# Performance work log

Hardware: AMD Instinct MI355X
Metric: run time of the kernel (lower is better)

## Reference

```python
import jax, jax.numpy as jnp
import numpy as np

BITS = 4
N_PACK = 32 // BITS  # int32 compression
GROUPSIZE = 128
MASK = (1 << BITS) - 1


def _unpack_int32(q, axis):
    """Unpack int32 tensor into N_PACK low-bit values along `axis`.
    Element j*N_PACK+e comes from bits [BITS*e, BITS*(e+1)) of packed word j."""
    parts = [ (q >> (BITS * e)) & MASK for e in range(N_PACK) ]
    u = jnp.stack(parts, axis=axis + 1)  # (..., P, N_PACK, ...)
    shape = list(q.shape)
    shape[axis] = shape[axis] * N_PACK
    return u.reshape(shape)


def setup_inputs() -> dict:
    key = jax.random.key(0)
    k1, k2, k3, k4, k5 = jax.random.split(key, 5)
    in_f, out_f = 4096, 12288
    tokens = 8192
    n_groups = in_f // GROUPSIZE  # 32
    x = jax.random.normal(k1, (tokens, in_f), dtype=jnp.float32)
    scales = jax.random.uniform(k2, (n_groups, out_f), dtype=jnp.float32) * 0.01 + 1e-3
    bias = jax.random.normal(k3, (out_f,), dtype=jnp.float32)
    qweight = jax.random.randint(k4, (in_f // N_PACK, out_f), jnp.iinfo(jnp.int32).min, jnp.iinfo(jnp.int32).max, dtype=jnp.int32)
    qzeros = jax.random.randint(k5, (n_groups, out_f // N_PACK), jnp.iinfo(jnp.int32).min, jnp.iinfo(jnp.int32).max, dtype=jnp.int32)
    return {"x": x, "scales": scales, "bias": bias, "qweight": qweight, "qzeros": qzeros}


def reference(x, scales, bias, qweight, qzeros):
    in_f = qweight.shape[0] * N_PACK
    out_f = qweight.shape[1]
    n_groups = scales.shape[0]
    # Unpack 4-bit weights along input-channel axis: (in_f, out_f), values 0..15
    w_int = _unpack_int32(qweight, axis=0).astype(scales.dtype)
    # Unpack zero points along output-channel axis; optimum format stores zp-1
    zp = (_unpack_int32(qzeros, axis=1) + 1).astype(scales.dtype)  # (n_groups, out_f)
    # Per-group dequant: group g covers input channels [g*GROUPSIZE, (g+1)*GROUPSIZE)
    w = (w_int.reshape(n_groups, GROUPSIZE, out_f) - zp[:, None, :]) * scales[:, None, :]
    w = w.reshape(in_f, out_f)
    # Linear: y = x @ W^T with W = w.T, i.e. x @ w
    return x @ w + bias
```

## Files before the change

### kernel.cpp

```cpp
#include <hip/hip_runtime.h>
#include <hip/hip_bf16.h>


typedef __attribute__((ext_vector_type(8))) short short8;
typedef __attribute__((ext_vector_type(4))) float f32x4;

__device__ __forceinline__ short f2bf(float f) {
  unsigned u = __float_as_uint(f);
  u += 0x7fffu + ((u >> 16) & 1u);
  return (short)(u >> 16);
}

__device__ __forceinline__ void gload_lds16(const void* g, void* l) {
  __builtin_amdgcn_global_load_lds(
      (const __attribute__((address_space(1))) void*)g,
      (__attribute__((address_space(3))) void*)l,
      16, 0, 0);
}

__device__ __forceinline__ void bar() {
  asm volatile("" ::: "memory");
  __builtin_amdgcn_s_barrier();
  asm volatile("" ::: "memory");
}
__device__ __forceinline__ void wait_vm8() {
  asm volatile("s_waitcnt vmcnt(8)" ::: "memory");
}
__device__ __forceinline__ void wait_vm4() {
  asm volatile("s_waitcnt vmcnt(4)" ::: "memory");
}
__device__ __forceinline__ void wait_vm0() {
  asm volatile("s_waitcnt vmcnt(0)" ::: "memory");
}

__global__ __launch_bounds__(256) void dequant_kernel(
    const int* __restrict__ qweight, const int* __restrict__ qzeros,
    const float* __restrict__ scales, short* __restrict__ Wt,
    int in_f, int out_f) {
  __shared__ __align__(16) short T[64][72];
  const int n0 = blockIdx.x * 64;
  const int k0 = blockIdx.y * 64;
  const int t = threadIdx.x;
  const int nl = t & 63;
  const int kw = t >> 6;
  const int n = n0 + nl;
  const int g = k0 >> 7;
  const float sc = scales[(size_t)g * out_f + n];
  const int zpw = qzeros[(size_t)g * (out_f >> 3) + (n >> 3)];
  const float zp = (float)(((zpw >> ((n & 7) * 4)) & 15) + 1);
  const float zs = zp * sc;
#pragma unroll
  for (int rr = 0; rr < 2; ++rr) {
    const int kwi = kw + rr * 4;
    const int w = qweight[(size_t)((k0 >> 3) + kwi) * out_f + n];
    short8 v;
#pragma unroll
    for (int e = 0; e < 8; ++e) {
      float f = (float)((w >> (4 * e)) & 15) * sc - zs;
      v[e] = f2bf(f);
    }
    *(short8*)&T[nl][kwi * 8] = v;
  }
  __syncthreads();
#pragma unroll
  for (int rr = 0; rr < 2; ++rr) {
    const int c = rr * 256 + t;
    const int row = c >> 3, ch = c & 7;
    *(short8*)&Wt[(size_t)(n0 + row) * in_f + k0 + ch * 8] =
        *(const short8*)&T[row][ch * 8];
  }
}

__global__ __launch_bounds__(256) void cvt_kernel(
    const float* __restrict__ x, short* __restrict__ xb, long n8) {
  long i = (long)blockIdx.x * blockDim.x + threadIdx.x;
  if (i >= n8) return;
  const float* src = x + i * 8;
  float4 a = *(const float4*)src;
  float4 b = *(const float4*)(src + 4);
  short8 v;
  v[0] = f2bf(a.x); v[1] = f2bf(a.y); v[2] = f2bf(a.z); v[3] = f2bf(a.w);
  v[4] = f2bf(b.x); v[5] = f2bf(b.y); v[6] = f2bf(b.z); v[7] = f2bf(b.w);
  *(short8*)(xb + i * 8) = v;
}

#define GBM 256
#define GBN 256

__global__ __launch_bounds__(512, 2) void gemm256_kernel(
    const short* __restrict__ A, const short* __restrict__ Bt,
    const float* __restrict__ bias, float* __restrict__ C,
    int M, int N, int K) {
  __shared__ __align__(16) char lds[4][32768];
  const int tid = threadIdx.x;
  const int nbx = N / GBN;
  const int nwg = gridDim.x;
  int bid = blockIdx.x;
  if ((nwg & 7) == 0) bid = (bid & 7) * (nwg >> 3) + (bid >> 3);
  const int bm = (bid / nbx) * GBM;
  const int bn = (bid % nbx) * GBN;

  const int wid = tid >> 6, lane = tid & 63;
  const int wr = wid >> 2, wc = wid & 3;
  const int lrow = lane & 15;
  const int lq = lane >> 4;

  const int P = K >> 5;

  int offA[2][4], offB[4];
#pragma unroll
  for (int mh = 0; mh < 2; ++mh)
#pragma unroll
    for (int i = 0; i < 4; ++i) {
      const int row = wr * 128 + mh * 64 + i * 16 + lrow;
      const int s = lq ^ ((row >> 1) & 3);
      offA[mh][i] = row * 64 + s * 16;
    }
#pragma unroll
  for (int j = 0; j < 4; ++j) {
    const int row = wc * 64 + j * 16 + lrow;
    const int s = lq ^ ((row >> 1) & 3);
    offB[j] = 16384 + row * 64 + s * 16;
  }

  const int c0 = tid, c1 = tid + 512;
  const int rA0 = c0 >> 2, qA0 = (c0 & 3) ^ ((rA0 >> 1) & 3);
  const int rA1 = c1 >> 2, qA1 = (c1 & 3) ^ ((rA1 >> 1) & 3);
  const short* srcA0 = A + (size_t)(bm + rA0) * K + qA0 * 8;
  const short* srcA1 = A + (size_t)(bm + rA1) * K + qA1 * 8;
  const short* srcB0 = Bt + (size_t)(bn + rA0) * K + qA0 * 8;
  const short* srcB1 = Bt + (size_t)(bn + rA1) * K + qA1 * 8;
  const int dA0 = c0 * 16, dA1 = c1 * 16;
  const int dB0 = 16384 + c0 * 16, dB1 = 16384 + c1 * 16;

  auto STAGE = [&](int slot, int h) {
    const int kof = h * 32;
    char* sb = &lds[slot][0];
    gload_lds16(srcA0 + kof, sb + dA0);
    gload_lds16(srcA1 + kof, sb + dA1);
    gload_lds16(srcB0 + kof, sb + dB0);
    gload_lds16(srcB1 + kof, sb + dB1);
  };

  f32x4 acc[8][4] = {};

  auto PHASE = [&](int p, bool doStage) {
    const char* sb = &lds[p & 3][0];
    short8 bf[4], af[4];
#pragma unroll
    for (int j = 0; j < 4; ++j) bf[j] = *(const short8*)(sb + offB[j]);
#pragma unroll
    for (int i = 0; i < 4; ++i) af[i] = *(const short8*)(sb + offA[0][i]);
    if (doStage) STAGE((p + 3) & 3, p + 3);
    __builtin_amdgcn_s_setprio(1);
#pragma unroll
    for (int i = 0; i < 4; ++i)
#pragma unroll
      for (int j = 0; j < 4; ++j)
        acc[i][j] = __builtin_amdgcn_mfma_f32_16x16x32_bf16(
            af[i], bf[j], acc[i][j], 0, 0, 0);
    __builtin_amdgcn_s_setprio(0);
    short8 af2[4];
#pragma unroll
    for (int i = 0; i < 4; ++i) af2[i] = *(const short8*)(sb + offA[1][i]);
    __builtin_amdgcn_s_setprio(1);
#pragma unroll
    for (int i = 0; i < 4; ++i)
#pragma unroll
      for (int j = 0; j < 4; ++j)
        acc[4 + i][j] = __builtin_amdgcn_mfma_f32_16x16x32_bf16(
            af2[i], bf[j], acc[4 + i][j], 0, 0, 0);
    __builtin_amdgcn_s_setprio(0);
  };

  STAGE(0, 0);
  STAGE(1, 1);
  STAGE(2, 2);

  for (int p = 0; p <= P - 4; ++p) {
    wait_vm8();
    bar();
    PHASE(p, true);
  }
  wait_vm8(); bar(); PHASE(P - 3, false);
  wait_vm4(); bar(); PHASE(P - 2, false);
  wait_vm0(); bar(); PHASE(P - 1, false);

  const int crow0 = bm + wr * 128 + (lane >> 4) * 4;
  const int ccol0 = bn + wc * 64 + (lane & 15);
#pragma unroll
  for (int j = 0; j < 4; ++j) {
    const float bv = bias[ccol0 + j * 16];
#pragma unroll
    for (int i = 0; i < 8; ++i) {
#pragma unroll
      for (int r = 0; r < 4; ++r) {
        C[(size_t)(crow0 + i * 16 + r) * N + ccol0 + j * 16] =
            acc[i][j][r] + bv;
      }
    }
  }
}

#define BM 128
#define BN 128
#define BK 64

template <bool A_BF16>
__global__ __launch_bounds__(256) void gemm_bias_kernel(
    const void* __restrict__ Av, const short* __restrict__ Bt,
    const float* __restrict__ bias, float* __restrict__ C,
    int M, int N, int K) {
  __shared__ __align__(16) short As[BM * BK];
  __shared__ __align__(16) short Bs[BN * BK];
  const int tid = threadIdx.x;
  const int bm = blockIdx.y * BM;
  const int bn = blockIdx.x * BN;
  const int wid = tid >> 6, lane = tid & 63;
  const int wr = wid >> 1, wc = wid & 1;
  const int lrow = lane & 15;
  const int lk = (lane >> 4) * 8;

  f32x4 acc[4][4] = {};

  for (int kt = 0; kt < K; kt += BK) {
    if constexpr (A_BF16) {
      const short* A = (const short*)Av;
#pragma unroll
      for (int r = 0; r < 4; ++r) {
        const int c = r * 256 + tid;
        const int row = c >> 3, ch = c & 7;
        gload_lds16(A + (size_t)(bm + row) * K + kt + ch * 8,
                    (char*)As + c * 16);
      }
    } else {
      const float* A = (const float*)Av;
#pragma unroll
      for (int r = 0; r < 4; ++r) {
        const int c = r * 256 + tid;
        const int row = c >> 3, ch = c & 7;
        const float* src = A + (size_t)(bm + row) * K + kt + ch * 8;
        float4 f0 = *(const float4*)src;
        float4 f1 = *(const float4*)(src + 4);
        short8 v;
        v[0] = f2bf(f0.x); v[1] = f2bf(f0.y); v[2] = f2bf(f0.z); v[3] = f2bf(f0.w);
        v[4] = f2bf(f1.x); v[5] = f2bf(f1.y); v[6] = f2bf(f1.z); v[7] = f2bf(f1.w);
        *(short8*)((char*)As + c * 16) = v;
      }
    }
#pragma unroll
    for (int r = 0; r < 4; ++r) {
      const int c = r * 256 + tid;
      const int row = c >> 3, ch = c & 7;
      gload_lds16(Bt + (size_t)(bn + row) * K + kt + ch * 8,
                  (char*)Bs + c * 16);
    }
    __syncthreads();
#pragma unroll
    for (int kk = 0; kk < 2; ++kk) {
      short8 af[4], bf[4];
#pragma unroll
      for (int i = 0; i < 4; ++i)
        af[i] = *(const short8*)&As[(wr * 64 + i * 16 + lrow) * BK + kk * 32 + lk];
#pragma unroll
      for (int j = 0; j < 4; ++j)
        bf[j] = *(const short8*)&Bs[(wc * 64 + j * 16 + lrow) * BK + kk * 32 + lk];
#pragma unroll
      for (int i = 0; i < 4; ++i)
#pragma unroll
        for (int j = 0; j < 4; ++j)
          acc[i][j] = __builtin_amdgcn_mfma_f32_16x16x32_bf16(
              af[i], bf[j], acc[i][j], 0, 0, 0);
    }
    __syncthreads();
  }

  const int crow0 = bm + wr * 64 + (lane >> 4) * 4;
  const int ccol0 = bn + wc * 64 + (lane & 15);
#pragma unroll
  for (int j = 0; j < 4; ++j) {
    const float bv = bias[ccol0 + j * 16];
#pragma unroll
    for (int i = 0; i < 4; ++i) {
#pragma unroll
      for (int r = 0; r < 4; ++r) {
        C[(size_t)(crow0 + i * 16 + r) * N + ccol0 + j * 16] = acc[i][j][r] + bv;
      }
    }
  }
}

__global__ __launch_bounds__(256) void naive_kernel(
    const float* __restrict__ x, const float* __restrict__ scales,
    const float* __restrict__ bias, const int* __restrict__ qw,
    const int* __restrict__ qz, float* __restrict__ out,
    int M, int K, int N) {
  long idx = (long)blockIdx.x * blockDim.x + threadIdx.x;
  if (idx >= (long)M * N) return;
  const int n = (int)(idx % N);
  const int m = (int)(idx / N);
  float acc = 0.f;
  for (int g = 0; g < K / 128; ++g) {
    const float sc = scales[(size_t)g * N + n];
    const float zp =
        (float)(((qz[(size_t)g * (N >> 3) + (n >> 3)] >> ((n & 7) * 4)) & 15) + 1);
    const float zs = zp * sc;
    for (int kw = 0; kw < 16; ++kw) {
      const int w = qw[(size_t)(g * 16 + kw) * N + n];
      const float* xp = &x[(size_t)m * K + g * 128 + kw * 8];
#pragma unroll
      for (int e = 0; e < 8; ++e)
        acc += xp[e] * ((float)((w >> (4 * e)) & 15) * sc - zs);
    }
  }
  out[idx] = acc + bias[n];
}

extern "C" void kernel_launch(void* const* d_in, const int* in_sizes, int n_in,
                              void* d_out, int out_size, void* d_ws,
                              size_t ws_size, hipStream_t stream) {
  const float* x = (const float*)d_in[0];
  const float* scales = (const float*)d_in[1];
  const float* bias = (const float*)d_in[2];
  const int* qweight = (const int*)d_in[3];
  const int* qzeros = (const int*)d_in[4];
  float* out = (float*)d_out;

  const int out_f = in_sizes[2];
  const int kwords = in_sizes[3] / out_f;
  const int in_f = kwords * 8;
  const int tokens = in_sizes[0] / in_f;
  const int M = tokens, K = in_f, N = out_f;

  const size_t wt_bytes = (size_t)K * N * sizeof(short);
  const size_t xb_bytes = (size_t)M * K * sizeof(short);

  const bool div128 = (M % BM == 0) && (N % BN == 0) && (K % BK == 0) &&
                      (K % 128 == 0) && (N % 64 == 0);
  const bool div256 = (M % GBM == 0) && (N % GBN == 0) && (K % 128 == 0) &&
                      (N % 64 == 0);

  if (div128 && ws_size >= wt_bytes + xb_bytes) {
    short* Wt = (short*)d_ws;
    short* xb = (short*)((char*)d_ws + wt_bytes);
    dequant_kernel<<<dim3(N / 64, K / 64), 256, 0, stream>>>(
        qweight, qzeros, scales, Wt, K, N);
    const long n8 = (long)M * K / 8;
    cvt_kernel<<<(int)((n8 + 255) / 256), 256, 0, stream>>>(x, xb, n8);
    if (div256) {
      gemm256_kernel<<<(M / GBM) * (N / GBN), 512, 0, stream>>>(
          xb, Wt, bias, out, M, N, K);
    } else {
      gemm_bias_kernel<true><<<dim3(N / BN, M / BM), 256, 0, stream>>>(
          xb, Wt, bias, out, M, N, K);
    }
  } else if (div128 && ws_size >= wt_bytes) {
    short* Wt = (short*)d_ws;
    dequant_kernel<<<dim3(N / 64, K / 64), 256, 0, stream>>>(
        qweight, qzeros, scales, Wt, K, N);
    gemm_bias_kernel<false><<<dim3(N / BN, M / BM), 256, 0, stream>>>(
        x, Wt, bias, out, M, N, K);
  } else {
    const long total = (long)M * N;
    naive_kernel<<<(int)((total + 255) / 256), 256, 0, stream>>>(
        x, scales, bias, qweight, qzeros, out, M, K, N);
  }
}
```

Before: 847.9 us.

## Prefetch next-stage LDS fragments into double-buffered registers during MFMAs

The GEMM main loop is restructured so that the B fragments and the first A half for step q+1 are read from LDS while the MFMAs of step q run. Two register sets alternate, with the loop manually unrolled by two. The barrier and vmcnt wait move to the end of each step, and the per-fragment offset arrays become one base address plus constant strides. This aims to hide LDS read latency behind matrix math, at the cost of more vector registers and a loop that assumes an even number of K steps.

Measured after the change: 866.1 us. 1.02x slower.

```diff
diff --git a/kernel.cpp b/kernel.cpp
--- a/kernel.cpp
+++ b/kernel.cpp
@@ -22,9 +22,6 @@
   asm volatile("" ::: "memory");
   __builtin_amdgcn_s_barrier();
   asm volatile("" ::: "memory");
-}
-__device__ __forceinline__ void wait_vm8() {
-  asm volatile("s_waitcnt vmcnt(8)" ::: "memory");
 }
 __device__ __forceinline__ void wait_vm4() {
   asm volatile("s_waitcnt vmcnt(4)" ::: "memory");
@@ -107,21 +104,12 @@
 
   const int P = K >> 5;
 
-  int offA[2][4], offB[4];
-#pragma unroll
-  for (int mh = 0; mh < 2; ++mh)
-#pragma unroll
-    for (int i = 0; i < 4; ++i) {
-      const int row = wr * 128 + mh * 64 + i * 16 + lrow;
-      const int s = lq ^ ((row >> 1) & 3);
-      offA[mh][i] = row * 64 + s * 16;
-    }
-#pragma unroll
-  for (int j = 0; j < 4; ++j) {
-    const int row = wc * 64 + j * 16 + lrow;
-    const int s = lq ^ ((row >> 1) & 3);
-    offB[j] = 16384 + row * 64 + s * 16;
-  }
+  const int rowA = wr * 128 + lrow;
+  const int sA = lq ^ ((rowA >> 1) & 3);
+  const int baseA = rowA * 64 + sA * 16;
+  const int rowB = wc * 64 + lrow;
+  const int sB = lq ^ ((rowB >> 1) & 3);
+  const int baseB = 16384 + rowB * 64 + sB * 16;
 
   const int c0 = tid, c1 = tid + 512;
   const int rA0 = c0 >> 2, qA0 = (c0 & 3) ^ ((rA0 >> 1) & 3);
@@ -144,47 +132,72 @@
 
   f32x4 acc[8][4] = {};
 
-  auto PHASE = [&](int p, bool doStage) {
-    const char* sb = &lds[p & 3][0];
-    short8 bf[4], af[4];
-#pragma unroll
-    for (int j = 0; j < 4; ++j) bf[j] = *(const short8*)(sb + offB[j]);
-#pragma unroll
-    for (int i = 0; i < 4; ++i) af[i] = *(const short8*)(sb + offA[0][i]);
-    if (doStage) STAGE((p + 3) & 3, p + 3);
+  auto rdB4 = [&](const char* sb, short8(&bf)[4]) {
+#pragma unroll
+    for (int j = 0; j < 4; ++j)
+      bf[j] = *(const short8*)(sb + baseB + j * 1024);
+  };
+  auto rdA_mh0 = [&](const char* sb, short8(&af)[4]) {
+#pragma unroll
+    for (int i = 0; i < 4; ++i)
+      af[i] = *(const short8*)(sb + baseA + i * 1024);
+  };
+  auto rdA_mh1 = [&](const char* sb, short8(&af)[4]) {
+#pragma unroll
+    for (int i = 0; i < 4; ++i)
+      af[i] = *(const short8*)(sb + baseA + 4096 + i * 1024);
+  };
+
+  auto BODY = [&](int q, short8(&afC)[4], short8(&bfC)[4], short8(&afN)[4],
+                  short8(&bfN)[4]) {
+    const char* sbC = &lds[q & 3][0];
+    short8 af2[4];
+    rdA_mh1(sbC, af2);
+    if (q + 1 < P) {
+      const char* sbN = &lds[(q + 1) & 3][0];
+      rdB4(sbN, bfN);
+      rdA_mh0(sbN, afN);
+    }
+    if (q + 3 < P) STAGE((q + 3) & 3, q + 3);
     __builtin_amdgcn_s_setprio(1);
 #pragma unroll
     for (int i = 0; i < 4; ++i)
 #pragma unroll
       for (int j = 0; j < 4; ++j)
         acc[i][j] = __builtin_amdgcn_mfma_f32_16x16x32_bf16(
-            af[i], bf[j], acc[i][j], 0, 0, 0);
+            afC[i], bfC[j], acc[i][j], 0, 0, 0);
     __builtin_amdgcn_s_setprio(0);
-    short8 af2[4];
-#pragma unroll
-    for (int i = 0; i < 4; ++i) af2[i] = *(const short8*)(sb + offA[1][i]);
     __builtin_amdgcn_s_setprio(1);
 #pragma unroll
     for (int i = 0; i < 4; ++i)
 #pragma unroll
       for (int j = 0; j < 4; ++j)
         acc[4 + i][j] = __builtin_amdgcn_mfma_f32_16x16x32_bf16(
-            af2[i], bf[j], acc[4 + i][j], 0, 0, 0);
+            af2[i], bfC[j], acc[4 + i][j], 0, 0, 0);
     __builtin_amdgcn_s_setprio(0);
-  };
+    if (q <= P - 4) {
+      wait_vm4();
+      bar();
+    } else if (q == P - 3) {
+      wait_vm0();
+      bar();
+    }
+  };
+
+  short8 afA[4], bfA[4], afB[4], bfB[4];
 
   STAGE(0, 0);
   STAGE(1, 1);
   STAGE(2, 2);
-
-  for (int p = 0; p <= P - 4; ++p) {
-    wait_vm8();
-    bar();
-    PHASE(p, true);
-  }
-  wait_vm8(); bar(); PHASE(P - 3, false);
-  wait_vm4(); bar(); PHASE(P - 2, false);
-  wait_vm0(); bar(); PHASE(P - 1, false);
+  wait_vm4();
+  bar();
+  rdB4(&lds[0][0], bfA);
+  rdA_mh0(&lds[0][0], afA);
+
+  for (int p = 0; p < P; p += 2) {
+    BODY(p, afA, bfA, afB, bfB);
+    BODY(p + 1, afB, bfB, afA, bfA);
+  }
 
   const int crow0 = bm + wr * 128 + (lane >> 4) * 4;
   const int ccol0 = bn + wc * 64 + (lane & 15);
```

## Fuse 4-bit weight dequantization into the 256x256 bf16 MFMA GEMM main loop

Applied to the files above, without the earlier changes.

The separate dequant kernel and its bf16 weight buffer are removed. The GEMM now streams packed int32 qweight tiles into LDS with 4-byte direct global-to-LDS loads. Each wave unpacks its nibbles in registers, applying the per-group scale and zero point loaded once per 128-wide K group, before issuing the MFMAs. This trades the global write and re-read of the dequantized weight matrix, plus one kernel launch, for extra VALU work inside the MFMA loop. That work is repeated by every M-block, and the smaller 4-byte loads may be less efficient.

Result: slower. 1.071 ms (+26.3%).

```diff
diff --git a/kernel.cpp b/kernel.cpp
--- a/kernel.cpp
+++ b/kernel.cpp
@@ -17,6 +17,12 @@
       (__attribute__((address_space(3))) void*)l,
       16, 0, 0);
 }
+__device__ __forceinline__ void gload_lds4(const void* g, void* l) {
+  __builtin_amdgcn_global_load_lds(
+      (const __attribute__((address_space(1))) void*)g,
+      (__attribute__((address_space(3))) void*)l,
+      4, 0, 0);
+}
 
 __device__ __forceinline__ void bar() {
   asm volatile("" ::: "memory");
@@ -31,6 +37,21 @@
 }
 __device__ __forceinline__ void wait_vm0() {
   asm volatile("s_waitcnt vmcnt(0)" ::: "memory");
+}
+
+__device__ __forceinline__ short8 dq8(int w, float sc, float zsc) {
+  const unsigned we = (unsigned)w & 0x0f0f0f0fu;
+  const unsigned wo = ((unsigned)w >> 4) & 0x0f0f0f0fu;
+  short8 r;
+  r[0] = f2bf(fmaf((float)(we & 0xffu), sc, zsc));
+  r[1] = f2bf(fmaf((float)(wo & 0xffu), sc, zsc));
+  r[2] = f2bf(fmaf((float)((we >> 8) & 0xffu), sc, zsc));
+  r[3] = f2bf(fmaf((float)((wo >> 8) & 0xffu), sc, zsc));
+  r[4] = f2bf(fmaf((float)((we >> 16) & 0xffu), sc, zsc));
+  r[5] = f2bf(fmaf((float)((wo >> 16) & 0xffu), sc, zsc));
+  r[6] = f2bf(fmaf((float)(we >> 24), sc, zsc));
+  r[7] = f2bf(fmaf((float)(wo >> 24), sc, zsc));
+  return r;
 }
 
 __global__ __launch_bounds__(256) void dequant_kernel(
@@ -87,11 +108,12 @@
 #define GBM 256
 #define GBN 256
 
-__global__ __launch_bounds__(512, 2) void gemm256_kernel(
-    const short* __restrict__ A, const short* __restrict__ Bt,
+__global__ __launch_bounds__(512, 2) void gemm_fused_kernel(
+    const short* __restrict__ A, const int* __restrict__ qweight,
+    const int* __restrict__ qzeros, const float* __restrict__ scales,
     const float* __restrict__ bias, float* __restrict__ C,
     int M, int N, int K) {
-  __shared__ __align__(16) char lds[4][32768];
+  __shared__ __align__(16) char lds[81920];
   const int tid = threadIdx.x;
   const int nbx = N / GBN;
   const int nwg = gridDim.x;
@@ -106,21 +128,17 @@
   const int lq = lane >> 4;
 
   const int P = K >> 5;
-
-  int offA[2][4], offB[4];
-#pragma unroll
-  for (int mh = 0; mh < 2; ++mh)
-#pragma unroll
-    for (int i = 0; i < 4; ++i) {
-      const int row = wr * 128 + mh * 64 + i * 16 + lrow;
-      const int s = lq ^ ((row >> 1) & 3);
-      offA[mh][i] = row * 64 + s * 16;
-    }
+  const int G = K >> 7;
+
+  const int rowA = wr * 128 + lrow;
+  const int sA = lq ^ ((rowA >> 1) & 3);
+  const int baseA = rowA * 64 + sA * 16;
+
+  int offBq[4];
 #pragma unroll
   for (int j = 0; j < 4; ++j) {
-    const int row = wc * 64 + j * 16 + lrow;
-    const int s = lq ^ ((row >> 1) & 3);
-    offB[j] = 16384 + row * 64 + s * 16;
+    const int n = wc * 64 + j * 16 + lrow;
+    offBq[j] = 65536 + (n * 4 + lq) * 4;
   }
 
   const int c0 = tid, c1 = tid + 512;
@@ -128,30 +146,59 @@
   const int rA1 = c1 >> 2, qA1 = (c1 & 3) ^ ((rA1 >> 1) & 3);
   const short* srcA0 = A + (size_t)(bm + rA0) * K + qA0 * 8;
   const short* srcA1 = A + (size_t)(bm + rA1) * K + qA1 * 8;
-  const short* srcB0 = Bt + (size_t)(bn + rA0) * K + qA0 * 8;
-  const short* srcB1 = Bt + (size_t)(bn + rA1) * K + qA1 * 8;
   const int dA0 = c0 * 16, dA1 = c1 * 16;
-  const int dB0 = 16384 + c0 * 16, dB1 = 16384 + c1 * 16;
-
-  auto STAGE = [&](int slot, int h) {
-    const int kof = h * 32;
-    char* sb = &lds[slot][0];
-    gload_lds16(srcA0 + kof, sb + dA0);
-    gload_lds16(srcA1 + kof, sb + dA1);
-    gload_lds16(srcB0 + kof, sb + dB0);
-    gload_lds16(srcB1 + kof, sb + dB1);
+
+  const int nB0 = c0 >> 2, kwB0 = c0 & 3;
+  const int nB1 = c1 >> 2, kwB1 = c1 & 3;
+  const int* srcB0 = qweight + (size_t)kwB0 * N + bn + nB0;
+  const int* srcB1 = qweight + (size_t)kwB1 * N + bn + nB1;
+  const int dB0 = 65536 + c0 * 4, dB1 = 65536 + c1 * 4;
+
+  auto STAGE = [&](int slot, int q) {
+    char* sa = &lds[slot * 16384];
+    gload_lds16(srcA0 + q * 32, sa + dA0);
+    gload_lds16(srcA1 + q * 32, sa + dA1);
+    char* sq = &lds[slot * 4096];
+    gload_lds4(srcB0 + (size_t)q * 4 * N, sq + dB0);
+    gload_lds4(srcB1 + (size_t)q * 4 * N, sq + dB1);
   };
 
+  float scN[4], scC[4], zscC[4];
+  int zwN[4];
+  const int shz = (lrow & 7) * 4;
+  auto LOADSZ = [&](int g) {
+#pragma unroll
+    for (int j = 0; j < 4; ++j) {
+      scN[j] = scales[(size_t)g * N + bn + wc * 64 + j * 16 + lrow];
+      zwN[j] = qzeros[(size_t)g * (N >> 3) + (bn >> 3) + wc * 8 + j * 2 +
+                      (lrow >> 3)];
+    }
+  };
+  auto UPDATE_SZ = [&]() {
+#pragma unroll
+    for (int j = 0; j < 4; ++j) {
+      scC[j] = scN[j];
+      const float zp = (float)(((zwN[j] >> shz) & 15) + 1);
+      zscC[j] = -zp * scC[j];
+    }
+  };
+
   f32x4 acc[8][4] = {};
 
-  auto PHASE = [&](int p, bool doStage) {
-    const char* sb = &lds[p & 3][0];
-    short8 bf[4], af[4];
-#pragma unroll
-    for (int j = 0; j < 4; ++j) bf[j] = *(const short8*)(sb + offB[j]);
-#pragma unroll
-    for (int i = 0; i < 4; ++i) af[i] = *(const short8*)(sb + offA[0][i]);
-    if (doStage) STAGE((p + 3) & 3, p + 3);
+  auto BODY = [&](int q, bool doStage) {
+    const int slot = q & 3;
+    const char* sa = &lds[slot * 16384];
+    const char* sq = &lds[slot * 4096];
+    int w[4];
+#pragma unroll
+    for (int j = 0; j < 4; ++j) w[j] = *(const int*)(sq + offBq[j]);
+    short8 af[4];
+#pragma unroll
+    for (int i = 0; i < 4; ++i) af[i] = *(const short8*)(sa + baseA + i * 1024);
+    if (doStage) STAGE((q + 3) & 3, q + 3);
+    short8 bf[4];
+#pragma unroll
+    for (int j = 0; j < 4; ++j) bf[j] = dq8(w[j], scC[j], zscC[j]);
     __builtin_amdgcn_s_setprio(1);
 #pragma unroll
     for (int i = 0; i < 4; ++i)
@@ -162,7 +209,8 @@
     __builtin_amdgcn_s_setprio(0);
     short8 af2[4];
 #pragma unroll
-    for (int i = 0; i < 4; ++i) af2[i] = *(const short8*)(sb + offA[1][i]);
+    for (int i = 0; i < 4; ++i)
+      af2[i] = *(const short8*)(sa + baseA + 4096 + i * 1024);
     __builtin_amdgcn_s_setprio(1);
 #pragma unroll
     for (int i = 0; i < 4; ++i)
@@ -173,18 +221,37 @@
     __builtin_amdgcn_s_setprio(0);
   };
 
+  LOADSZ(0);
   STAGE(0, 0);
   STAGE(1, 1);
   STAGE(2, 2);
-
-  for (int p = 0; p <= P - 4; ++p) {
-    wait_vm8();
-    bar();
-    PHASE(p, true);
-  }
-  wait_vm8(); bar(); PHASE(P - 3, false);
-  wait_vm4(); bar(); PHASE(P - 2, false);
-  wait_vm0(); bar(); PHASE(P - 1, false);
+  wait_vm4();
+  bar();
+
+  for (int g = 0; g < G - 1; ++g) {
+    const int q0 = 4 * g;
+    UPDATE_SZ();
+    BODY(q0, true);
+    wait_vm8(); bar();
+    BODY(q0 + 1, true);
+    wait_vm8(); bar();
+    BODY(q0 + 2, true);
+    wait_vm8(); bar();
+    LOADSZ(g + 1);
+    BODY(q0 + 3, true);
+    wait_vm4(); bar();
+  }
+  {
+    const int q0 = P - 4;
+    UPDATE_SZ();
+    BODY(q0, true);
+    wait_vm8(); bar();
+    BODY(q0 + 1, false);
+    wait_vm4(); bar();
+    BODY(q0 + 2, false);
+    wait_vm0(); bar();
+    BODY(q0 + 3, false);
+  }
 
   const int crow0 = bm + wr * 128 + (lane >> 4) * 4;
   const int ccol0 = bn + wc * 64 + (lane & 15);
@@ -337,23 +404,23 @@
 
   const bool div128 = (M % BM == 0) && (N % BN == 0) && (K % BK == 0) &&
                       (K % 128 == 0) && (N % 64 == 0);
-  const bool div256 = (M % GBM == 0) && (N % GBN == 0) && (K % 128 == 0) &&
-                      (N % 64 == 0);
-
-  if (div128 && ws_size >= wt_bytes + xb_bytes) {
+  const bool div256 = (M % GBM == 0) && (N % GBN == 0) && (K % 128 == 0);
+
+  if (div256 && ws_size >= xb_bytes) {
+    short* xb = (short*)d_ws;
+    const long n8 = (long)M * K / 8;
+    cvt_kernel<<<(int)((n8 + 255) / 256), 256, 0, stream>>>(x, xb, n8);
+    gemm_fused_kernel<<<(M / GBM) * (N / GBN), 512, 0, stream>>>(
+        xb, qweight, qzeros, scales, bias, out, M, N, K);
+  } else if (div128 && ws_size >= wt_bytes + xb_bytes) {
     short* Wt = (short*)d_ws;
     short* xb = (short*)((char*)d_ws + wt_bytes);
     dequant_kernel<<<dim3(N / 64, K / 64), 256, 0, stream>>>(
         qweight, qzeros, scales, Wt, K, N);
     const long n8 = (long)M * K / 8;
     cvt_kernel<<<(int)((n8 + 255) / 256), 256, 0, stream>>>(x, xb, n8);
-    if (div256) {
-      gemm256_kernel<<<(M / GBM) * (N / GBN), 512, 0, stream>>>(
-          xb, Wt, bias, out, M, N, K);
-    } else {
-      gemm_bias_kernel<true><<<dim3(N / BN, M / BM), 256, 0, stream>>>(
-          xb, Wt, bias, out, M, N, K);
-    }
+    gemm_bias_kernel<true><<<dim3(N / BN, M / BM), 256, 0, stream>>>(
+        xb, Wt, bias, out, M, N, K);
   } else if (div128 && ws_size >= wt_bytes) {
     short* Wt = (short*)d_ws;
     dequant_kernel<<<dim3(N / 64, K / 64), 256, 0, stream>>>(
```

## Shrink GEMM tile to 128x256 with 4 waves and triple-buffered LDS

Applied to the files above, without the earlier changes.

Replaces the 256x256, 512-thread GEMM with a 128x256 tile run by 256 threads (4 waves, each covering all 128 rows and 64 columns). The LDS ring drops from four 32KB stages to three 24KB stages, and the wait/barrier now sits after each compute body. This lowers LDS use per block and doubles the grid, aiming for more resident blocks and better load balance. In exchange, A/B operand reuse per block falls, raising global and L2 traffic for the B operand.

Result: slower. 1.146 ms (+35.2%).

```diff
diff --git a/kernel.cpp b/kernel.cpp
--- a/kernel.cpp
+++ b/kernel.cpp
@@ -23,11 +23,8 @@
   __builtin_amdgcn_s_barrier();
   asm volatile("" ::: "memory");
 }
-__device__ __forceinline__ void wait_vm8() {
-  asm volatile("s_waitcnt vmcnt(8)" ::: "memory");
-}
-__device__ __forceinline__ void wait_vm4() {
-  asm volatile("s_waitcnt vmcnt(4)" ::: "memory");
+__device__ __forceinline__ void wait_vm6() {
+  asm volatile("s_waitcnt vmcnt(6)" ::: "memory");
 }
 __device__ __forceinline__ void wait_vm0() {
   asm volatile("s_waitcnt vmcnt(0)" ::: "memory");
@@ -84,14 +81,14 @@
   *(short8*)(xb + i * 8) = v;
 }
 
-#define GBM 256
+#define GBM 128
 #define GBN 256
 
-__global__ __launch_bounds__(512, 2) void gemm256_kernel(
+__global__ __launch_bounds__(256, 2) void gemm128x256_kernel(
     const short* __restrict__ A, const short* __restrict__ Bt,
     const float* __restrict__ bias, float* __restrict__ C,
     int M, int N, int K) {
-  __shared__ __align__(16) char lds[4][32768];
+  __shared__ __align__(16) char lds[3 * 24576];
   const int tid = threadIdx.x;
   const int nbx = N / GBN;
   const int nwg = gridDim.x;
@@ -100,58 +97,53 @@
   const int bm = (bid / nbx) * GBM;
   const int bn = (bid % nbx) * GBN;
 
-  const int wid = tid >> 6, lane = tid & 63;
-  const int wr = wid >> 2, wc = wid & 3;
+  const int wc = tid >> 6;
+  const int lane = tid & 63;
   const int lrow = lane & 15;
   const int lq = lane >> 4;
 
   const int P = K >> 5;
 
-  int offA[2][4], offB[4];
-#pragma unroll
-  for (int mh = 0; mh < 2; ++mh)
-#pragma unroll
-    for (int i = 0; i < 4; ++i) {
-      const int row = wr * 128 + mh * 64 + i * 16 + lrow;
-      const int s = lq ^ ((row >> 1) & 3);
-      offA[mh][i] = row * 64 + s * 16;
-    }
-#pragma unroll
-  for (int j = 0; j < 4; ++j) {
-    const int row = wc * 64 + j * 16 + lrow;
-    const int s = lq ^ ((row >> 1) & 3);
-    offB[j] = 16384 + row * 64 + s * 16;
-  }
-
-  const int c0 = tid, c1 = tid + 512;
-  const int rA0 = c0 >> 2, qA0 = (c0 & 3) ^ ((rA0 >> 1) & 3);
-  const int rA1 = c1 >> 2, qA1 = (c1 & 3) ^ ((rA1 >> 1) & 3);
+  const int swz = (lq ^ ((lrow >> 1) & 3)) * 16;
+  const int baseA = lrow * 64 + swz;
+  const int baseB = 8192 + (wc * 64 + lrow) * 64 + swz;
+
+  const int cA0 = tid, cA1 = tid + 256;
+  const int rA0 = cA0 >> 2, qA0 = (cA0 & 3) ^ ((rA0 >> 1) & 3);
+  const int rA1 = cA1 >> 2, qA1 = (cA1 & 3) ^ ((rA1 >> 1) & 3);
   const short* srcA0 = A + (size_t)(bm + rA0) * K + qA0 * 8;
   const short* srcA1 = A + (size_t)(bm + rA1) * K + qA1 * 8;
-  const short* srcB0 = Bt + (size_t)(bn + rA0) * K + qA0 * 8;
-  const short* srcB1 = Bt + (size_t)(bn + rA1) * K + qA1 * 8;
-  const int dA0 = c0 * 16, dA1 = c1 * 16;
-  const int dB0 = 16384 + c0 * 16, dB1 = 16384 + c1 * 16;
-
-  auto STAGE = [&](int slot, int h) {
-    const int kof = h * 32;
-    char* sb = &lds[slot][0];
+  const int dA0 = cA0 * 16, dA1 = cA1 * 16;
+
+  const short* srcB[4];
+  int dB[4];
+#pragma unroll
+  for (int r = 0; r < 4; ++r) {
+    const int c = tid + 256 * r;
+    const int row = c >> 2, qq = (c & 3) ^ ((row >> 1) & 3);
+    srcB[r] = Bt + (size_t)(bn + row) * K + qq * 8;
+    dB[r] = 8192 + c * 16;
+  }
+
+  auto STAGE = [&](int slot, int q) {
+    char* sb = &lds[slot * 24576];
+    const int kof = q * 32;
     gload_lds16(srcA0 + kof, sb + dA0);
     gload_lds16(srcA1 + kof, sb + dA1);
-    gload_lds16(srcB0 + kof, sb + dB0);
-    gload_lds16(srcB1 + kof, sb + dB1);
+#pragma unroll
+    for (int r = 0; r < 4; ++r) gload_lds16(srcB[r] + kof, sb + dB[r]);
   };
 
   f32x4 acc[8][4] = {};
 
-  auto PHASE = [&](int p, bool doStage) {
-    const char* sb = &lds[p & 3][0];
+  auto BODY = [&](int sl, int qn, bool doStage) {
+    const char* sb = &lds[sl * 24576];
     short8 bf[4], af[4];
 #pragma unroll
-    for (int j = 0; j < 4; ++j) bf[j] = *(const short8*)(sb + offB[j]);
-#pragma unroll
-    for (int i = 0; i < 4; ++i) af[i] = *(const short8*)(sb + offA[0][i]);
-    if (doStage) STAGE((p + 3) & 3, p + 3);
+    for (int j = 0; j < 4; ++j) bf[j] = *(const short8*)(sb + baseB + j * 1024);
+#pragma unroll
+    for (int i = 0; i < 4; ++i) af[i] = *(const short8*)(sb + baseA + i * 1024);
+    if (doStage) STAGE(sl == 0 ? 2 : sl - 1, qn);
     __builtin_amdgcn_s_setprio(1);
 #pragma unroll
     for (int i = 0; i < 4; ++i)
@@ -162,7 +154,8 @@
     __builtin_amdgcn_s_setprio(0);
     short8 af2[4];
 #pragma unroll
-    for (int i = 0; i < 4; ++i) af2[i] = *(const short8*)(sb + offA[1][i]);
+    for (int i = 0; i < 4; ++i)
+      af2[i] = *(const short8*)(sb + baseA + 4096 + i * 1024);
     __builtin_amdgcn_s_setprio(1);
 #pragma unroll
     for (int i = 0; i < 4; ++i)
@@ -175,18 +168,23 @@
 
   STAGE(0, 0);
   STAGE(1, 1);
-  STAGE(2, 2);
-
-  for (int p = 0; p <= P - 4; ++p) {
-    wait_vm8();
-    bar();
-    PHASE(p, true);
-  }
-  wait_vm8(); bar(); PHASE(P - 3, false);
-  wait_vm4(); bar(); PHASE(P - 2, false);
-  wait_vm0(); bar(); PHASE(P - 1, false);
-
-  const int crow0 = bm + wr * 128 + (lane >> 4) * 4;
+  wait_vm6();
+  bar();
+
+  int sl = 0;
+  for (int q = 0; q < P; ++q) {
+    BODY(sl, q + 2, q + 2 < P);
+    if (q < P - 2) {
+      wait_vm6();
+      bar();
+    } else if (q == P - 2) {
+      wait_vm0();
+      bar();
+    }
+    sl = (sl == 2) ? 0 : sl + 1;
+  }
+
+  const int crow0 = bm + (lane >> 4) * 4;
   const int ccol0 = bn + wc * 64 + (lane & 15);
 #pragma unroll
   for (int j = 0; j < 4; ++j) {
@@ -337,8 +335,7 @@
 
   const bool div128 = (M % BM == 0) && (N % BN == 0) && (K % BK == 0) &&
                       (K % 128 == 0) && (N % 64 == 0);
-  const bool div256 = (M % GBM == 0) && (N % GBN == 0) && (K % 128 == 0) &&
-                      (N % 64 == 0);
+  const bool divR7 = (M % GBM == 0) && (N % GBN == 0) && (K % 128 == 0);
 
   if (div128 && ws_size >= wt_bytes + xb_bytes) {
     short* Wt = (short*)d_ws;
@@ -347,8 +344,8 @@
         qweight, qzeros, scales, Wt, K, N);
     const long n8 = (long)M * K / 8;
     cvt_kernel<<<(int)((n8 + 255) / 256), 256, 0, stream>>>(x, xb, n8);
-    if (div256) {
-      gemm256_kernel<<<(M / GBM) * (N / GBN), 512, 0, stream>>>(
+    if (divR7) {
+      gemm128x256_kernel<<<(M / GBM) * (N / GBN), 256, 0, stream>>>(
           xb, Wt, bias, out, M, N, K);
     } else {
       gemm_bias_kernel<true><<<dim3(N / BN, M / BM), 256, 0, stream>>>(
```
